# Optimization experiments

Measured on AMD Instinct MI355X. Metric: run time of the kernel, lower is better.

The kernel has to match this reference:

```python
import jax, jax.numpy as jnp
import numpy as np

# dims: B frames, L residues, E embed, C comp_size, K kernel, NL layers, V vocab
B, L, E, C, K, NL, V = 64, 256, 128, 16, 5, 4, 21
STEP = 0.1


def setup_inputs() -> dict:
    key = jax.random.key(0)
    ks = jax.random.split(key, 9)
    aa_array = jax.random.randint(ks[0], (B, L), 0, V)
    bb_coords = jax.random.normal(ks[1], (B, L, 3), dtype=jnp.float32)
    emb = jax.random.normal(ks[2], (V, E), dtype=jnp.float32) * 0.05
    conv_w = jax.random.normal(ks[3], (NL, E, E, K), dtype=jnp.float32) * (1.0 / np.sqrt(E * K))
    conv_b = jax.random.normal(ks[4], (NL, E), dtype=jnp.float32) * 0.01
    t1_w = jax.random.normal(ks[5], (E * C, E), dtype=jnp.float32) * (1.0 / np.sqrt(E))
    t1_b = jax.random.normal(ks[6], (E * C,), dtype=jnp.float32) * 0.01
    t2_w = jax.random.normal(ks[7], (3 * C, 3), dtype=jnp.float32) * (1.0 / np.sqrt(3.0))
    t2_b = jax.random.normal(ks[8], (3 * C,), dtype=jnp.float32) * 0.01
    return {"aa_array": aa_array, "bb_coords": bb_coords, "emb": emb,
            "conv_w": conv_w, "conv_b": conv_b,
            "t1_w": t1_w, "t1_b": t1_b, "t2_w": t2_w, "t2_b": t2_b}


def _forward(aa_array, bb_coords, emb, conv_w, conv_b, t1_w, t1_b, t2_w, t2_b):
    # --- model.call: embed + residual conv stack with tanh ---
    h = emb[aa_array].transpose(0, 2, 1)  # (B, E, L)
    for i in range(NL):
        y = jax.lax.conv_general_dilated(
            h, conv_w[i], window_strides=(1,), padding='SAME',
            dimension_numbers=('NCH', 'OIH', 'NCH'))
        h = jnp.tanh(h + y + conv_b[i][None, :, None])
    x = h.transpose(0, 2, 1)  # (B, L, E)

    # --- pairwise coordinate message passing ---
    xx = bb_coords[:, :, None] - bb_coords[:, None, :]        # (B, L, L, 3)
    x2 = (x @ t1_w.T + t1_b).reshape(B, L, E, C)              # (B, L, E, C)
    # xc[b,c,i,j] = sum_e x[b,i,e] * x2[b,j,e,c]
    scores = jnp.einsum('bie,bjec->bcij', x, x2)              # (B, C, L, L)
    sm = jax.nn.softmax(scores, axis=1)                       # softmax over C

    # torch: pv = t2(xx).reshape(B,L,L,3,C); vd[b,a,k] = sum_{d,c} pv[b,a,d,k,c]*sm[b,c,d,a]
    # fused form (same math, avoids materializing pv of shape (B,L,L,3,C)):
    W2 = t2_w.reshape(3, C, 3)   # (k, c, m)
    b2 = t2_b.reshape(3, C)      # (k, c)
    s = jnp.einsum('badm,bcda->bcam', xx, sm)                 # (B, C, L, 3)
    vd = (jnp.einsum('kcm,bcam->bak', W2, s)
          + jnp.einsum('kc,bca->bak', b2, sm.sum(axis=2)))    # (B, L, 3)

    new_bb = bb_coords + STEP * vd
    mse = jnp.square(new_bb[1:] - bb_coords[:-1]).sum(-1).mean(1)  # (B-1,)
    return mse


def reference(aa_array, bb_coords, emb, conv_w, conv_b, t1_w, t1_b, t2_w, t2_b):
    return _forward(aa_array, bb_coords, emb, conv_w, conv_b, t1_w, t1_b, t2_w, t2_b)
```

## Files before the change

kernel.cpp:

```cpp
#include <hip/hip_runtime.h>

#define B_ 64
#define L_ 256
#define E_ 128
#define C_ 16
#define K_ 5
#define NL_ 4
#define STEP_ 0.1f
#define LOG2E_ 1.4426950408889634f

typedef __bf16 bfh;
typedef __attribute__((ext_vector_type(8))) __bf16 bf16x8;
typedef __attribute__((ext_vector_type(4))) float f32x4;
typedef __attribute__((ext_vector_type(16))) float f32x16;

#define SWZ(r) (((r) ^ ((r) >> 4)) & 15)

__global__ void k_prep_w(const float* __restrict__ w, bfh* __restrict__ wT) {
  int i = blockIdx.x * 256 + threadIdx.x;
  if (i >= NL_ * K_ * E_ * E_) return;
  int ii = i & 127;
  int rest = i >> 7;
  int o = rest & 127;
  int rest2 = rest >> 7;
  int k = rest2 % K_;
  int lay = rest2 / K_;
  wT[i] = (bfh)w[(((size_t)lay * E_ + o) * E_ + ii) * K_ + k];
}

__global__ void k_prep_t1(const float* __restrict__ t1w, bfh* __restrict__ t1wb) {
  int i = blockIdx.x * 256 + threadIdx.x;
  if (i < 2048 * 128) t1wb[i] = (bfh)(t1w[i] * LOG2E_);
}

__global__ __launch_bounds__(512, 4) void k_conv0(const int* __restrict__ aa,
                                                  const float* __restrict__ emb,
                                                  const bfh* __restrict__ wT,
                                                  const float* __restrict__ bias,
                                                  bfh* __restrict__ xout) {
  __shared__ __align__(16) char hs[36 * 256];
  const int b = blockIdx.y;
  const int lb = blockIdx.x * 32;
  const int t = threadIdx.x;

  for (int s = t; s < 36 * 16; s += 512) {
    int row = s >> 4, ch = s & 15;
    int lp = lb + row - 2;
    uint4 pk = {0, 0, 0, 0};
    if (lp >= 0 && lp < L_) {
      int idx = aa[b * L_ + lp];
      float4 f0 = *(const float4*)(emb + (size_t)idx * E_ + ch * 8);
      float4 f1 = *(const float4*)(emb + (size_t)idx * E_ + ch * 8 + 4);
      union { bfh h[8]; uint4 u; } cv;
      cv.h[0] = (bfh)f0.x; cv.h[1] = (bfh)f0.y; cv.h[2] = (bfh)f0.z; cv.h[3] = (bfh)f0.w;
      cv.h[4] = (bfh)f1.x; cv.h[5] = (bfh)f1.y; cv.h[6] = (bfh)f1.z; cv.h[7] = (bfh)f1.w;
      pk = cv.u;
    }
    *(uint4*)(hs + row * 256 + ((ch ^ (row & 7)) << 4)) = pk;
  }
  __syncthreads();

  const int wv = t >> 6, lane = t & 63;
  const int c16 = lane & 15, kg = lane >> 4;
  const int msub = wv & 1;
  const int nq = wv >> 1;

#pragma unroll
  for (int ntl = 0; ntl < 2; ++ntl) {
    const int n0 = nq * 32 + ntl * 16;
    f32x4 acc = {0.f, 0.f, 0.f, 0.f};
#pragma unroll
    for (int k = 0; k < K_; ++k) {
      const bfh* bp = wT + ((size_t)(k * E_ + n0 + c16)) * E_ + kg * 8;
      bf16x8 b0 = *(const bf16x8*)(bp);
      bf16x8 b1 = *(const bf16x8*)(bp + 32);
      bf16x8 b2 = *(const bf16x8*)(bp + 64);
      bf16x8 b3 = *(const bf16x8*)(bp + 96);
      const int row = msub * 16 + c16 + k;
      bf16x8 a0 = *(const bf16x8*)(hs + row * 256 + (((0 * 4 + kg) ^ (row & 7)) << 4));
      bf16x8 a1 = *(const bf16x8*)(hs + row * 256 + (((1 * 4 + kg) ^ (row & 7)) << 4));
      bf16x8 a2 = *(const bf16x8*)(hs + row * 256 + (((2 * 4 + kg) ^ (row & 7)) << 4));
      bf16x8 a3 = *(const bf16x8*)(hs + row * 256 + (((3 * 4 + kg) ^ (row & 7)) << 4));
      acc = __builtin_amdgcn_mfma_f32_16x16x32_bf16(a0, b0, acc, 0, 0, 0);
      acc = __builtin_amdgcn_mfma_f32_16x16x32_bf16(a1, b1, acc, 0, 0, 0);
      acc = __builtin_amdgcn_mfma_f32_16x16x32_bf16(a2, b2, acc, 0, 0, 0);
      acc = __builtin_amdgcn_mfma_f32_16x16x32_bf16(a3, b3, acc, 0, 0, 0);
    }
    const int o = n0 + c16;
    const float bo = bias[o];
#pragma unroll
    for (int r = 0; r < 4; ++r) {
      int lrow = msub * 16 + kg * 4 + r;
      int srow = lrow + 2;
      float res = (float)*(const bfh*)(hs + srow * 256 +
                                       (((o >> 3) ^ (srow & 7)) << 4) + (o & 7) * 2);
      float v = acc[r] + res + bo;
      float ex = __expf(2.f * v);
      float th = 1.f - 2.f / (ex + 1.f);
      xout[((size_t)b * L_ + lb + lrow) * E_ + o] = (bfh)th;
    }
  }
}

__global__ __launch_bounds__(512, 4) void k_conv(const bfh* __restrict__ xin,
                                                 const bfh* __restrict__ wT,
                                                 const float* __restrict__ bias,
                                                 bfh* __restrict__ xout) {
  __shared__ __align__(16) char hs[36 * 256];
  const int b = blockIdx.y;
  const int lb = blockIdx.x * 32;
  const int t = threadIdx.x;

  for (int s = t; s < 36 * 16; s += 512) {
    int row = s >> 4, ch = s & 15;
    int lp = lb + row - 2;
    uint4 z = {0, 0, 0, 0};
    uint4 v = (lp >= 0 && lp < L_)
                  ? *(const uint4*)(xin + ((size_t)b * L_ + lp) * E_ + ch * 8)
                  : z;
    *(uint4*)(hs + row * 256 + ((ch ^ (row & 7)) << 4)) = v;
  }
  __syncthreads();

  const int wv = t >> 6, lane = t & 63;
  const int c16 = lane & 15, kg = lane >> 4;
  const int msub = wv & 1;
  const int nq = wv >> 1;

#pragma unroll
  for (int ntl = 0; ntl < 2; ++ntl) {
    const int n0 = nq * 32 + ntl * 16;
    f32x4 acc = {0.f, 0.f, 0.f, 0.f};
#pragma unroll
    for (int k = 0; k < K_; ++k) {
      const bfh* bp = wT + ((size_t)(k * E_ + n0 + c16)) * E_ + kg * 8;
      bf16x8 b0 = *(const bf16x8*)(bp);
      bf16x8 b1 = *(const bf16x8*)(bp + 32);
      bf16x8 b2 = *(const bf16x8*)(bp + 64);
      bf16x8 b3 = *(const bf16x8*)(bp + 96);
      const int row = msub * 16 + c16 + k;
      bf16x8 a0 = *(const bf16x8*)(hs + row * 256 + (((0 * 4 + kg) ^ (row & 7)) << 4));
      bf16x8 a1 = *(const bf16x8*)(hs + row * 256 + (((1 * 4 + kg) ^ (row & 7)) << 4));
      bf16x8 a2 = *(const bf16x8*)(hs + row * 256 + (((2 * 4 + kg) ^ (row & 7)) << 4));
      bf16x8 a3 = *(const bf16x8*)(hs + row * 256 + (((3 * 4 + kg) ^ (row & 7)) << 4));
      acc = __builtin_amdgcn_mfma_f32_16x16x32_bf16(a0, b0, acc, 0, 0, 0);
      acc = __builtin_amdgcn_mfma_f32_16x16x32_bf16(a1, b1, acc, 0, 0, 0);
      acc = __builtin_amdgcn_mfma_f32_16x16x32_bf16(a2, b2, acc, 0, 0, 0);
      acc = __builtin_amdgcn_mfma_f32_16x16x32_bf16(a3, b3, acc, 0, 0, 0);
    }
    const int o = n0 + c16;
    const float bo = bias[o];
#pragma unroll
    for (int r = 0; r < 4; ++r) {
      int lrow = msub * 16 + kg * 4 + r;
      int srow = lrow + 2;
      float res = (float)*(const bfh*)(hs + srow * 256 +
                                       (((o >> 3) ^ (srow & 7)) << 4) + (o & 7) * 2);
      float v = acc[r] + res + bo;
      float ex = __expf(2.f * v);
      float th = 1.f - 2.f / (ex + 1.f);
      xout[((size_t)b * L_ + lb + lrow) * E_ + o] = (bfh)th;
    }
  }
}

__global__ __launch_bounds__(512, 4) void k_conv_last(const bfh* __restrict__ xin,
                                                      const bfh* __restrict__ wT,
                                                      const float* __restrict__ bias,
                                                      bfh* __restrict__ xTg) {
  __shared__ __align__(16) char hs[36 * 256];
  const int b = blockIdx.y;
  const int lb = blockIdx.x * 32;
  const int dt = blockIdx.x;
  const int t = threadIdx.x;

  for (int s = t; s < 36 * 16; s += 512) {
    int row = s >> 4, ch = s & 15;
    int lp = lb + row - 2;
    uint4 z = {0, 0, 0, 0};
    uint4 v = (lp >= 0 && lp < L_)
                  ? *(const uint4*)(xin + ((size_t)b * L_ + lp) * E_ + ch * 8)
                  : z;
    *(uint4*)(hs + row * 256 + ((ch ^ (row & 7)) << 4)) = v;
  }
  __syncthreads();

  const int wv = t >> 6, lane = t & 63;
  const int c16 = lane & 15, kg = lane >> 4;
  const int msub = wv & 1;
  const int nq = wv >> 1;

#pragma unroll
  for (int ntl = 0; ntl < 2; ++ntl) {
    const int n0 = nq * 32 + ntl * 16;
    f32x4 acc = {0.f, 0.f, 0.f, 0.f};
#pragma unroll
    for (int k = 0; k < K_; ++k) {
      const bfh* bp = wT + ((size_t)(k * E_ + n0 + c16)) * E_ + kg * 8;
      bf16x8 b0 = *(const bf16x8*)(bp);
      bf16x8 b1 = *(const bf16x8*)(bp + 32);
      bf16x8 b2 = *(const bf16x8*)(bp + 64);
      bf16x8 b3 = *(const bf16x8*)(bp + 96);
      const int row = msub * 16 + c16 + k;
      bf16x8 a0 = *(const bf16x8*)(hs + row * 256 + (((0 * 4 + kg) ^ (row & 7)) << 4));
      bf16x8 a1 = *(const bf16x8*)(hs + row * 256 + (((1 * 4 + kg) ^ (row & 7)) << 4));
      bf16x8 a2 = *(const bf16x8*)(hs + row * 256 + (((2 * 4 + kg) ^ (row & 7)) << 4));
      bf16x8 a3 = *(const bf16x8*)(hs + row * 256 + (((3 * 4 + kg) ^ (row & 7)) << 4));
      acc = __builtin_amdgcn_mfma_f32_16x16x32_bf16(a0, b0, acc, 0, 0, 0);
      acc = __builtin_amdgcn_mfma_f32_16x16x32_bf16(a1, b1, acc, 0, 0, 0);
      acc = __builtin_amdgcn_mfma_f32_16x16x32_bf16(a2, b2, acc, 0, 0, 0);
      acc = __builtin_amdgcn_mfma_f32_16x16x32_bf16(a3, b3, acc, 0, 0, 0);
    }
    const int o = n0 + c16;
    const int kkp = nq * 2 + ntl;
    const int hic = c16 >> 3;
    const int e7 = c16 & 7;
    const float bo = bias[o];
#pragma unroll
    for (int r = 0; r < 4; ++r) {
      int lrow = msub * 16 + kg * 4 + r;
      int srow = lrow + 2;
      float res = (float)*(const bfh*)(hs + srow * 256 +
                                       (((o >> 3) ^ (srow & 7)) << 4) + (o & 7) * 2);
      float v = acc[r] + res + bo;
      float ex = __expf(2.f * v);
      float th = 1.f - 2.f / (ex + 1.f);
      size_t el = ((((size_t)b * 8 + dt) * 8 + kkp) * 2 + hic) * 256 + lrow * 8 + e7;
      xTg[el] = (bfh)th;
    }
  }
}

__global__ __launch_bounds__(512, 2) void k_x2(const bfh* __restrict__ xTg,
                                               const bfh* __restrict__ t1wb,
                                               const float* __restrict__ t1b,
                                               bfh* __restrict__ x2g,
                                               int bBase) {
  __shared__ __align__(16) char smem[65536 + 2 * 8192];
  char* XF = smem;
  const int b_loc = blockIdx.y;
  const int b = bBase + b_loc;
  const int ne = blockIdx.x;
  const int t = threadIdx.x;
  const int wv = t >> 6, lane = t & 63;
  const int c16 = lane & 15, kg = lane >> 4;

#pragma unroll
  for (int i = 0; i < 8; ++i) {
    int c = t + i * 512;
    int l31 = c & 31, hi5 = (c >> 5) & 1, kk = (c >> 6) & 7, dt = c >> 9;
    int row = dt * 32 + l31;
    int ch = (kk * 2 + hi5) ^ SWZ(row);
    *(uint4*)(XF + row * 256 + (ch << 4)) =
        *(const uint4*)(xTg + (size_t)b * 32768 + (size_t)c * 8);
  }
  __syncthreads();

  bf16x8 bf[2][4];
  float bias[2];
#pragma unroll
  for (int j = 0; j < 2; ++j) {
    const int e = ne * 16 + wv * 2 + j;
    const int n = e * 16 + c16;
#pragma unroll
    for (int kk = 0; kk < 4; ++kk)
      bf[j][kk] = *(const bf16x8*)(t1wb + (size_t)n * 128 + kk * 32 + kg * 8);
    bias[j] = t1b[n] * LOG2E_;
  }

#pragma unroll 1
  for (int st = 0; st < 16; ++st) {
    char* sc = smem + 65536 + (st & 1) * 8192;
    bf16x8 a1[4];
    const int rowa = st * 16 + c16;
#pragma unroll
    for (int kk = 0; kk < 4; ++kk)
      a1[kk] = *(const bf16x8*)(XF + rowa * 256 + (((kk * 4 + kg) ^ SWZ(rowa)) << 4));
    f32x4 acc0 = {0.f, 0.f, 0.f, 0.f};
    f32x4 acc1 = {0.f, 0.f, 0.f, 0.f};
#pragma unroll
    for (int kk = 0; kk < 4; ++kk) {
      acc0 = __builtin_amdgcn_mfma_f32_16x16x32_bf16(a1[kk], bf[0][kk], acc0, 0, 0, 0);
      acc1 = __builtin_amdgcn_mfma_f32_16x16x32_bf16(a1[kk], bf[1][kk], acc1, 0, 0, 0);
    }
#pragma unroll
    for (int r = 0; r < 4; ++r) {
      int a = kg * 4 + r;
      int m5 = (c16 & 3) | ((a & 1) << 2) | ((c16 >> 2) << 3);
      int row = (a >> 1) * 32 + m5;
      union { bfh h; ushort s; } lo, hi2;
      lo.h = (bfh)(acc0[r] + bias[0]);
      hi2.h = (bfh)(acc1[r] + bias[1]);
      unsigned pk = (unsigned)lo.s | ((unsigned)hi2.s << 16);
      *(unsigned*)(sc + row * 32 + (((wv) ^ ((row >> 2) & 7)) << 2)) = pk;
    }
    __syncthreads();
    {
      const int m32 = t & 31;
      const int eo = (t >> 5) & 1;
      const int mb = t >> 6;
      const int row = mb * 32 + m32;
      uint4 v;
      unsigned* vp = (unsigned*)&v;
#pragma unroll
      for (int jj = 0; jj < 4; ++jj) {
        int j2 = eo * 4 + jj;
        vp[jj] = *(const unsigned*)(sc + row * 32 + ((j2 ^ ((row >> 2) & 7)) << 2));
      }
      size_t el = (((size_t)(b_loc * 128 + st * 8 + mb)) * 16 + ne * 2 + eo) * 256 + m32 * 8;
      *(uint4*)(x2g + el) = v;
    }
  }
}

__global__ __launch_bounds__(512, 2) void k_pair(
    const bfh* __restrict__ xTg,
    const float* __restrict__ bb,
    const bfh* __restrict__ x2g,
    const float* __restrict__ t2w,
    const float* __restrict__ t2b,
    float* __restrict__ nbb,
    int bBase) {
  __shared__ __align__(16) float bbs[L_ * 3];
  const int t = threadIdx.x;
  const unsigned u = blockIdx.x;
  const int b_loc = (u & 7) | ((u >> 7) << 3);
  const int atile = (u >> 3) & 15;
  const int b = bBase + b_loc;
  const int lane = t & 63;
  const int wv = t >> 6;
  const int l31 = lane & 31;
  const int hi = lane >> 5;

  if (t < 192) ((float4*)bbs)[t] = ((const float4*)(bb + b * (L_ * 3)))[t];
  __syncthreads();

  bf16x8 afr[8];
  const bfh* abase = x2g + ((size_t)(b_loc * 128 + atile * 8 + wv)) * 4096 + l31 * 8;
#pragma unroll
  for (int kk = 0; kk < 8; ++kk)
    afr[kk] = *(const bf16x8*)(abase + (kk * 2 + hi) * 256);

  const int aglob = atile * 16 + 2 * wv + hi;
  const float bax0 = bbs[aglob * 3 + 0];
  const float bax1 = bbs[aglob * 3 + 1];
  const float bax2 = bbs[aglob * 3 + 2];

  float accX[16], accY[16], accZ[16], accS[16];
#pragma unroll
  for (int q = 0; q < 16; ++q) { accX[q] = 0.f; accY[q] = 0.f; accZ[q] = 0.f; accS[q] = 0.f; }

  const bfh* xb = xTg + (size_t)b * 32768 + hi * 256 + l31 * 8;
  bf16x8 bcur[8], bnxt[8];
#pragma unroll
  for (int kk = 0; kk < 8; ++kk) bcur[kk] = *(const bf16x8*)(xb + kk * 512);

#pragma unroll
  for (int dt = 0; dt < 8; ++dt) {
    if (dt < 7) {
#pragma unroll
      for (int kk = 0; kk < 8; ++kk)
        bnxt[kk] = *(const bf16x8*)(xb + (dt + 1) * 4096 + kk * 512);
    }
    f32x16 acc0, acc1;
#pragma unroll
    for (int q = 0; q < 16; ++q) { acc0[q] = 0.f; acc1[q] = 0.f; }
#pragma unroll
    for (int kk = 0; kk < 4; ++kk) {
      acc0 = __builtin_amdgcn_mfma_f32_32x32x16_bf16(afr[2 * kk], bcur[2 * kk], acc0, 0, 0, 0);
      acc1 = __builtin_amdgcn_mfma_f32_32x32x16_bf16(afr[2 * kk + 1], bcur[2 * kk + 1], acc1, 0, 0, 0);
    }
    const int d = dt * 32 + l31;
    const float dx = bax0 - bbs[d * 3 + 0];
    const float dy = bax1 - bbs[d * 3 + 1];
    const float dz = bax2 - bbs[d * 3 + 2];
    float p[16];
#pragma unroll
    for (int q = 0; q < 16; ++q) p[q] = exp2f(acc0[q] + acc1[q]);
    const float s0 = (p[0] + p[1]) + (p[2] + p[3]);
    const float s1 = (p[4] + p[5]) + (p[6] + p[7]);
    const float s2 = (p[8] + p[9]) + (p[10] + p[11]);
    const float s3 = (p[12] + p[13]) + (p[14] + p[15]);
    const float S = (s0 + s1) + (s2 + s3);
    const float inv = __builtin_amdgcn_rcpf(S);
#pragma unroll
    for (int q = 0; q < 16; ++q) {
      const float uu = p[q] * inv;
      accS[q] += uu;
      accX[q] = fmaf(uu, dx, accX[q]);
      accY[q] = fmaf(uu, dy, accY[q]);
      accZ[q] = fmaf(uu, dz, accZ[q]);
    }
#pragma unroll
    for (int kk = 0; kk < 8; ++kk) bcur[kk] = bnxt[kk];
  }

  float vk[3] = {0.f, 0.f, 0.f};
#pragma unroll
  for (int c = 0; c < 16; ++c) {
#pragma unroll
    for (int k = 0; k < 3; ++k) {
      const float* w2 = t2w + (k * C_ + c) * 3;
      vk[k] += w2[0] * accX[c] + w2[1] * accY[c] + w2[2] * accZ[c] +
               t2b[k * C_ + c] * accS[c];
    }
  }
#pragma unroll
  for (int m = 1; m <= 16; m <<= 1) {
    vk[0] += __shfl_xor(vk[0], m);
    vk[1] += __shfl_xor(vk[1], m);
    vk[2] += __shfl_xor(vk[2], m);
  }
  if (l31 == 0) {
#pragma unroll
    for (int k = 0; k < 3; ++k)
      nbb[(size_t)(b * L_ + aglob) * 3 + k] = bbs[aglob * 3 + k] + STEP_ * vk[k];
  }
}

__global__ void k_mse(const float* __restrict__ nbb, const float* __restrict__ bb,
                      float* __restrict__ out) {
  const int b = blockIdx.x;
  const int t = threadIdx.x;
  const float* pn = nbb + ((b + 1) * L_ + t) * 3;
  const float* pb = bb + (b * L_ + t) * 3;
  const float dx = pn[0] - pb[0];
  const float dy = pn[1] - pb[1];
  const float dz = pn[2] - pb[2];
  float v = dx * dx + dy * dy + dz * dz;
  for (int o = 32; o > 0; o >>= 1) v += __shfl_down(v, o);
  __shared__ float wsum[4];
  if ((t & 63) == 0) wsum[t >> 6] = v;
  __syncthreads();
  if (t == 0) out[b] = (wsum[0] + wsum[1] + wsum[2] + wsum[3]) * (1.0f / L_);
}

extern "C" void kernel_launch(void* const* d_in, const int* in_sizes, int n_in,
                              void* d_out, int out_size, void* d_ws, size_t ws_size,
                              hipStream_t stream) {
  const int* aa = (const int*)d_in[0];
  const float* bb = (const float*)d_in[1];
  const float* emb = (const float*)d_in[2];
  const float* conv_w = (const float*)d_in[3];
  const float* conv_b = (const float*)d_in[4];
  const float* t1w = (const float*)d_in[5];
  const float* t1b = (const float*)d_in[6];
  const float* t2w = (const float*)d_in[7];
  const float* t2b = (const float*)d_in[8];
  float* out = (float*)d_out;

  char* ws = (char*)d_ws;
  bfh* xA = (bfh*)ws;
  bfh* xTg = (bfh*)(ws + 4194304);
  bfh* t1wb = (bfh*)(ws + 8388608);
  bfh* wT = (bfh*)(ws + 8912896);
  float* nbb = (float*)(ws + 9568256);
  bfh* x2g = (bfh*)(ws + 10485760);
  bfh* xB = (bfh*)(ws + 10485760);

  k_prep_t1<<<1024, 256, 0, stream>>>(t1w, t1wb);
  k_prep_w<<<(NL_ * K_ * E_ * E_ + 255) / 256, 256, 0, stream>>>(conv_w, wT);

  k_conv0<<<dim3(L_ / 32, B_), 512, 0, stream>>>(aa, emb, wT + (size_t)0 * K_ * E_ * E_,
                                                 conv_b + 0 * E_, xB);
  k_conv<<<dim3(L_ / 32, B_), 512, 0, stream>>>(xB, wT + (size_t)1 * K_ * E_ * E_,
                                                conv_b + 1 * E_, xA);
  k_conv<<<dim3(L_ / 32, B_), 512, 0, stream>>>(xA, wT + (size_t)2 * K_ * E_ * E_,
                                                conv_b + 2 * E_, xB);
  k_conv_last<<<dim3(L_ / 32, B_), 512, 0, stream>>>(xB, wT + (size_t)3 * K_ * E_ * E_,
                                                     conv_b + 3 * E_, xTg);

  const size_t need1 = 10485760ull + 67108864ull;
  if (ws_size >= need1) {
    k_x2<<<dim3(8, B_), 512, 0, stream>>>(xTg, t1wb, t1b, x2g, 0);
    k_pair<<<B_ * 16, 512, 0, stream>>>(xTg, bb, x2g, t2w, t2b, nbb, 0);
  } else {
    for (int pass = 0; pass < 2; ++pass) {
      const int bBase = pass * 32;
      k_x2<<<dim3(8, 32), 512, 0, stream>>>(xTg, t1wb, t1b, x2g, bBase);
      k_pair<<<512, 512, 0, stream>>>(xTg, bb, x2g, t2w, t2b, nbb, bBase);
    }
  }

  k_mse<<<B_ - 1, 256, 0, stream>>>(nbb, bb, out);
}
```

Baseline: 163.2 us.

## Split pair kernel over residue halves and reduce partials in MSE kernel

The pair kernel now splits the d (column residue) dimension into two halves handled by separate 256-thread blocks. This quadruples the grid and halves the serial tile loop per block, with the aim of better occupancy and latency hiding. Each block writes a partial displacement vector, and the MSE kernel sums the two halves and applies the step update. The softmax-weighted accumulation also folds the reciprocal into the coordinate deltas so each accumulate is a single FMA. The cost is duplicated per-block setup (A-fragment loads, bb staging) and an extra partial buffer round-trip.

```diff
diff --git a/kernel.cpp b/kernel.cpp
--- a/kernel.cpp
+++ b/kernel.cpp
@@ -313,19 +313,21 @@
   }
 }
 
-__global__ __launch_bounds__(512, 2) void k_pair(
+__global__ __launch_bounds__(256, 4) void k_pair(
     const bfh* __restrict__ xTg,
     const float* __restrict__ bb,
     const bfh* __restrict__ x2g,
     const float* __restrict__ t2w,
     const float* __restrict__ t2b,
-    float* __restrict__ nbb,
+    float* __restrict__ vkp,
     int bBase) {
   __shared__ __align__(16) float bbs[L_ * 3];
   const int t = threadIdx.x;
   const unsigned u = blockIdx.x;
-  const int b_loc = (u & 7) | ((u >> 7) << 3);
-  const int atile = (u >> 3) & 15;
+  const int b_loc = (u & 7) | ((u >> 9) << 3);
+  const int inner = (u >> 3) & 63;
+  const int atile = inner >> 1;
+  const int dh = inner & 1;
   const int b = bBase + b_loc;
   const int lane = t & 63;
   const int wv = t >> 6;
@@ -336,12 +338,12 @@
   __syncthreads();
 
   bf16x8 afr[8];
-  const bfh* abase = x2g + ((size_t)(b_loc * 128 + atile * 8 + wv)) * 4096 + l31 * 8;
+  const bfh* abase = x2g + ((size_t)(b_loc * 128 + atile * 4 + wv)) * 4096 + l31 * 8;
 #pragma unroll
   for (int kk = 0; kk < 8; ++kk)
     afr[kk] = *(const bf16x8*)(abase + (kk * 2 + hi) * 256);
 
-  const int aglob = atile * 16 + 2 * wv + hi;
+  const int aglob = atile * 8 + 2 * wv + hi;
   const float bax0 = bbs[aglob * 3 + 0];
   const float bax1 = bbs[aglob * 3 + 1];
   const float bax2 = bbs[aglob * 3 + 2];
@@ -353,14 +355,16 @@
   const bfh* xb = xTg + (size_t)b * 32768 + hi * 256 + l31 * 8;
   bf16x8 bcur[8], bnxt[8];
 #pragma unroll
-  for (int kk = 0; kk < 8; ++kk) bcur[kk] = *(const bf16x8*)(xb + kk * 512);
-
-#pragma unroll
-  for (int dt = 0; dt < 8; ++dt) {
-    if (dt < 7) {
+  for (int kk = 0; kk < 8; ++kk)
+    bcur[kk] = *(const bf16x8*)(xb + (size_t)(dh * 4) * 4096 + kk * 512);
+
+#pragma unroll
+  for (int dt = 0; dt < 4; ++dt) {
+    const int dtg = dh * 4 + dt;
+    if (dt < 3) {
 #pragma unroll
       for (int kk = 0; kk < 8; ++kk)
-        bnxt[kk] = *(const bf16x8*)(xb + (dt + 1) * 4096 + kk * 512);
+        bnxt[kk] = *(const bf16x8*)(xb + (size_t)(dtg + 1) * 4096 + kk * 512);
     }
     f32x16 acc0, acc1;
 #pragma unroll
@@ -370,7 +374,7 @@
       acc0 = __builtin_amdgcn_mfma_f32_32x32x16_bf16(afr[2 * kk], bcur[2 * kk], acc0, 0, 0, 0);
       acc1 = __builtin_amdgcn_mfma_f32_32x32x16_bf16(afr[2 * kk + 1], bcur[2 * kk + 1], acc1, 0, 0, 0);
     }
-    const int d = dt * 32 + l31;
+    const int d = dtg * 32 + l31;
     const float dx = bax0 - bbs[d * 3 + 0];
     const float dy = bax1 - bbs[d * 3 + 1];
     const float dz = bax2 - bbs[d * 3 + 2];
@@ -383,13 +387,13 @@
     const float s3 = (p[12] + p[13]) + (p[14] + p[15]);
     const float S = (s0 + s1) + (s2 + s3);
     const float inv = __builtin_amdgcn_rcpf(S);
+    const float dxn = dx * inv, dyn = dy * inv, dzn = dz * inv;
 #pragma unroll
     for (int q = 0; q < 16; ++q) {
-      const float uu = p[q] * inv;
-      accS[q] += uu;
-      accX[q] = fmaf(uu, dx, accX[q]);
-      accY[q] = fmaf(uu, dy, accY[q]);
-      accZ[q] = fmaf(uu, dz, accZ[q]);
+      accS[q] = fmaf(p[q], inv, accS[q]);
+      accX[q] = fmaf(p[q], dxn, accX[q]);
+      accY[q] = fmaf(p[q], dyn, accY[q]);
+      accZ[q] = fmaf(p[q], dzn, accZ[q]);
     }
 #pragma unroll
     for (int kk = 0; kk < 8; ++kk) bcur[kk] = bnxt[kk];
@@ -414,20 +418,24 @@
   if (l31 == 0) {
 #pragma unroll
     for (int k = 0; k < 3; ++k)
-      nbb[(size_t)(b * L_ + aglob) * 3 + k] = bbs[aglob * 3 + k] + STEP_ * vk[k];
-  }
-}
-
-__global__ void k_mse(const float* __restrict__ nbb, const float* __restrict__ bb,
+      vkp[(((size_t)b * 2 + dh) * L_ + aglob) * 3 + k] = vk[k];
+  }
+}
+
+__global__ void k_mse(const float* __restrict__ vkp, const float* __restrict__ bb,
                       float* __restrict__ out) {
   const int b = blockIdx.x;
   const int t = threadIdx.x;
-  const float* pn = nbb + ((b + 1) * L_ + t) * 3;
-  const float* pb = bb + (b * L_ + t) * 3;
-  const float dx = pn[0] - pb[0];
-  const float dy = pn[1] - pb[1];
-  const float dz = pn[2] - pb[2];
-  float v = dx * dx + dy * dy + dz * dz;
+  const int bp1 = b + 1;
+  float v = 0.f;
+#pragma unroll
+  for (int k = 0; k < 3; ++k) {
+    float vd = vkp[(((size_t)bp1 * 2 + 0) * L_ + t) * 3 + k] +
+               vkp[(((size_t)bp1 * 2 + 1) * L_ + t) * 3 + k];
+    float nb = bb[((size_t)bp1 * L_ + t) * 3 + k] + STEP_ * vd;
+    float d = nb - bb[((size_t)b * L_ + t) * 3 + k];
+    v += d * d;
+  }
   for (int o = 32; o > 0; o >>= 1) v += __shfl_down(v, o);
   __shared__ float wsum[4];
   if ((t & 63) == 0) wsum[t >> 6] = v;
@@ -454,7 +462,7 @@
   bfh* xTg = (bfh*)(ws + 4194304);
   bfh* t1wb = (bfh*)(ws + 8388608);
   bfh* wT = (bfh*)(ws + 8912896);
-  float* nbb = (float*)(ws + 9568256);
+  float* vkp = (float*)(ws + 9568256);
   bfh* x2g = (bfh*)(ws + 10485760);
   bfh* xB = (bfh*)(ws + 10485760);
 
@@ -473,14 +481,14 @@
   const size_t need1 = 10485760ull + 67108864ull;
   if (ws_size >= need1) {
     k_x2<<<dim3(8, B_), 512, 0, stream>>>(xTg, t1wb, t1b, x2g, 0);
-    k_pair<<<B_ * 16, 512, 0, stream>>>(xTg, bb, x2g, t2w, t2b, nbb, 0);
+    k_pair<<<B_ * 64, 256, 0, stream>>>(xTg, bb, x2g, t2w, t2b, vkp, 0);
   } else {
     for (int pass = 0; pass < 2; ++pass) {
       const int bBase = pass * 32;
       k_x2<<<dim3(8, 32), 512, 0, stream>>>(xTg, t1wb, t1b, x2g, bBase);
-      k_pair<<<512, 512, 0, stream>>>(xTg, bb, x2g, t2w, t2b, nbb, bBase);
-    }
-  }
-
-  k_mse<<<B_ - 1, 256, 0, stream>>>(nbb, bb, out);
-}
+      k_pair<<<32 * 64, 256, 0, stream>>>(xTg, bb, x2g, t2w, t2b, vkp, bBase);
+    }
+  }
+
+  k_mse<<<B_ - 1, 256, 0, stream>>>(vkp, bb, out);
+}
```

New measurement: 166.7 us. 1.02x slower.
